# Kernel optimization log

Measured on AMD Instinct MI355X. Metric: run time of the kernel, lower is better.

Reference implementation:

```python
import jax, jax.numpy as jnp
import numpy as np

N_SAMPLES = 2048
BURN_IN = 128
STEP_SIZE = 0.1
D = 512   # walker dimension
H = 1024  # wavefunction MLP hidden width


def setup_inputs() -> dict:
    key = jax.random.key(0)
    k0, k1, k2 = jax.random.split(key, 3)
    x0 = jax.random.normal(k0, (1, D), dtype=jnp.float32)
    W1 = jax.random.normal(k1, (D, H), dtype=jnp.float32) / np.float32(np.sqrt(D))
    b1 = jnp.zeros((H,), dtype=jnp.float32)
    W2 = jax.random.normal(k2, (H, 1), dtype=jnp.float32) / np.float32(np.sqrt(H))
    b2 = jnp.zeros((1,), dtype=jnp.float32)
    return {"x0": x0, "W1": W1, "b1": b1, "W2": W2, "b2": b2}


def _model(x, W1, b1, W2, b2):
    # wavefunction MLP: [1, D] -> [1, 1]
    return jnp.tanh(x @ W1 + b1) @ W2 + b2


def reference(x0, W1, b1, W2, b2):
    def psi2(x):
        # model(x).pow(2)[0] -> shape [1]
        return (_model(x, W1, b1, W2, b2) ** 2)[0]

    def mh_step(x, k):
        k_noise, k_unif = jax.random.split(k)
        x_new = x + jax.random.normal(k_noise, x.shape, dtype=x.dtype) * STEP_SIZE
        p_new = psi2(x_new)
        p_old = psi2(x)
        ratio = jnp.minimum(p_new / (p_old + 1e-12), 1.0)          # clamp(max=1.0)
        u = jax.random.uniform(k_unif, ratio.shape, dtype=x.dtype)
        accept = (u < ratio).astype(x.dtype)[:, None]               # [1, 1]
        x = accept * x_new + (1.0 - accept) * x
        return x, x[0]  # carry chain state, record sample row [D]

    keys = jax.random.split(jax.random.key(1), N_SAMPLES + BURN_IN)
    _, traj = jax.lax.scan(mh_step, x0, keys)   # traj: [N+BURN_IN, D]
    return traj[BURN_IN:]                        # [N_SAMPLES, D]
```

## Files before the change

kernel.cpp:

```cpp
#include <hip/hip_runtime.h>
#include <stdint.h>
#include <math.h>


#define T_TOTAL 2176
#define NBURN   128
#define DDIM    512
#define HDIM    1024
#define DONE_FLAG 0x13572468u

__device__ __forceinline__ uint2 tf2x32(uint32_t k0, uint32_t k1,
                                        uint32_t x0, uint32_t x1) {
  uint32_t ks2 = k0 ^ k1 ^ 0x1BD11BDAu;
  x0 += k0; x1 += k1;
#define TF_R(r) { x0 += x1; x1 = (x1 << (r)) | (x1 >> (32 - (r))); x1 ^= x0; }
  TF_R(13) TF_R(15) TF_R(26) TF_R(6)
  x0 += k1;  x1 += ks2 + 1u;
  TF_R(17) TF_R(29) TF_R(16) TF_R(24)
  x0 += ks2; x1 += k0 + 2u;
  TF_R(13) TF_R(15) TF_R(26) TF_R(6)
  x0 += k0;  x1 += k1 + 3u;
  TF_R(17) TF_R(29) TF_R(16) TF_R(24)
  x0 += k1;  x1 += ks2 + 4u;
  TF_R(13) TF_R(15) TF_R(26) TF_R(6)
  x0 += ks2; x1 += k0 + 5u;
#undef TF_R
  return make_uint2(x0, x1);
}

__device__ __forceinline__ float erfinv_xla(float x) {
  float w = -log1pf(-x * x);
  float p;
  if (w < 5.0f) {
    w = w - 2.5f;
    p = 2.81022636e-08f;
    p = fmaf(p, w, 3.43273939e-07f);
    p = fmaf(p, w, -3.5233877e-06f);
    p = fmaf(p, w, -4.39150654e-06f);
    p = fmaf(p, w, 0.00021858087f);
    p = fmaf(p, w, -0.00125372503f);
    p = fmaf(p, w, -0.00417768164f);
    p = fmaf(p, w, 0.246640727f);
    p = fmaf(p, w, 1.50140941f);
  } else {
    w = sqrtf(w) - 3.0f;
    p = -0.000200214257f;
    p = fmaf(p, w, 0.000100950558f);
    p = fmaf(p, w, 0.00134934322f);
    p = fmaf(p, w, -0.00367342844f);
    p = fmaf(p, w, 0.00573950773f);
    p = fmaf(p, w, -0.0076224613f);
    p = fmaf(p, w, 0.00943887047f);
    p = fmaf(p, w, 1.00167406f);
    p = fmaf(p, w, 2.83297682f);
  }
  return p * x;
}

__device__ __forceinline__ float normal_from_bits(uint32_t bits) {
  const float lo = -0.99999994f;
  float u01 = __uint_as_float(0x3f800000u | (bits >> 9)) - 1.0f;
  float v = u01 * 2.0f + lo;
  v = fmaxf(lo, v);
  return 1.41421356237309515f * erfinv_xla(v);
}

__device__ __forceinline__ float tanh_fast(float x) {
  float a = x * 2.88539008177792681472f;
#if __has_builtin(__builtin_amdgcn_exp2f)
  float e = __builtin_amdgcn_exp2f(a);
#else
  float e = exp2f(a);
#endif
  float r = __builtin_amdgcn_rcpf(e + 1.0f);
  return fmaf(-2.0f, r, 1.0f);
}

__global__ void __launch_bounds__(256) rng_kernel(const float* __restrict__ x0,
                                                  float* __restrict__ A,
                                                  float* __restrict__ U) {
  const uint32_t t = blockIdx.x;
  const int tid = threadIdx.x;
  uint2 kt = tf2x32(0u, 1u, 0u, t);
  uint2 kn = tf2x32(kt.x, kt.y, 0u, 0u);
  uint2 e0 = tf2x32(kn.x, kn.y, 0u, (uint32_t)tid);
  uint2 e1 = tf2x32(kn.x, kn.y, 0u, (uint32_t)(tid + 256));
  float n0 = normal_from_bits(e0.x ^ e0.y);
  float n1 = normal_from_bits(e1.x ^ e1.y);
  float* Arow = A + (size_t)(t + 1) * DDIM;
  Arow[tid]       = n0 * 0.1f;
  Arow[tid + 256] = n1 * 0.1f;
  if (tid == 0) {
    uint2 ku = tf2x32(kt.x, kt.y, 0u, 1u);
    uint2 eu = tf2x32(ku.x, ku.y, 0u, 0u);
    U[t] = __uint_as_float(0x3f800000u | ((eu.x ^ eu.y) >> 9)) - 1.0f;
  }
  if (t == 0) {
    A[tid]       = x0[tid];
    A[tid + 256] = x0[tid + 256];
  }
}

__global__ void __launch_bounds__(512) gemm_kernel(const float* __restrict__ A,
                                                   const float* __restrict__ W1,
                                                   float* __restrict__ Z,
                                                   int nrows) {
  const int r0 = blockIdx.x * 8;
  const int t  = threadIdx.x;
  const int c0 = t, c1 = t + 512;
  double acc[8][2];
#pragma unroll
  for (int r = 0; r < 8; ++r) { acc[r][0] = 0.0; acc[r][1] = 0.0; }
  for (int d = 0; d < 512; d += 4) {
    double wA[4], wB[4];
#pragma unroll
    for (int j = 0; j < 4; ++j) {
      wA[j] = (double)W1[(size_t)(d + j) * 1024 + c0];
      wB[j] = (double)W1[(size_t)(d + j) * 1024 + c1];
    }
#pragma unroll
    for (int r = 0; r < 8; ++r) {
      int rr = r0 + r; if (rr >= nrows) rr = nrows - 1;
      const float4 a4 = *(const float4*)(A + (size_t)rr * 512 + d);
      double a0 = (double)a4.x, a1 = (double)a4.y;
      double a2 = (double)a4.z, a3 = (double)a4.w;
      acc[r][0] += (a0 * wA[0] + a1 * wA[1]) + (a2 * wA[2] + a3 * wA[3]);
      acc[r][1] += (a0 * wB[0] + a1 * wB[1]) + (a2 * wB[2] + a3 * wB[3]);
    }
  }
  const int rmax = (nrows - r0 < 8) ? (nrows - r0) : 8;
  for (int r = 0; r < rmax; ++r) {
    Z[(size_t)(r0 + r) * 1024 + c0] = (float)acc[r][0];
    Z[(size_t)(r0 + r) * 1024 + c1] = (float)acc[r][1];
  }
}

#define DPP_ADD(v, ctrl)                                                     \
  v += __int_as_float(__builtin_amdgcn_update_dpp(                           \
      0, __float_as_int(v), (ctrl), 0xF, 0xF, true))

__device__ __forceinline__ float wave_reduce_to_last(float v) {
  DPP_ADD(v, 0xB1);
  DPP_ADD(v, 0x4E);
  DPP_ADD(v, 0x141);
  DPP_ADD(v, 0x140);
  DPP_ADD(v, 0x142);
  DPP_ADD(v, 0x143);
  return v;
}

#define BAR() asm volatile("s_waitcnt lgkmcnt(0)\n\ts_barrier" ::: "memory")

__global__ void __launch_bounds__(256) chain_kernel(
    const float* __restrict__ Z, const float* __restrict__ A,
    const float* __restrict__ U, const float* __restrict__ x0,
    const float* __restrict__ b1, const float* __restrict__ W2,
    const float* __restrict__ b2, float* __restrict__ out,
    unsigned* __restrict__ flag) {
  const int tid = threadIdx.x;

  if (blockIdx.x != 0) {
    float acc = (float)tid * 1.0e-6f;
    for (int i = 0; i < 4000; ++i) {
#pragma unroll
      for (int j = 0; j < 256; ++j) acc = fmaf(acc, 0.99999988f, 1.0e-7f);
      unsigned f = __hip_atomic_load(flag, __ATOMIC_RELAXED,
                                     __HIP_MEMORY_SCOPE_AGENT);
      if (f == DONE_FLAG) break;
    }
    if (acc == 123456.75f && tid == 1023) out[0] = acc;
    return;
  }

  const int lane = tid & 63;
  const int wid = tid >> 6;
  __shared__ __align__(16) float wsum[2][4];
  __shared__ float Uld[T_TOTAL];

  const float4* Zv = (const float4*)Z;
  const float2* Av = (const float2*)A;

  for (int i = tid; i < T_TOTAL; i += 256) Uld[i] = U[i];

  const float4 w2v = ((const float4*)W2)[tid];
  const float4 b1v = ((const float4*)b1)[tid];
  const float b2v = b2[0];

  float4 z0r = Zv[tid];
  float4 zr1 = Zv[256 + tid];
  float4 zS0 = Zv[512 + tid];
  float4 zS1 = Zv[768 + tid];
  float2 dS0 = Av[256 + tid];
  float2 dS1 = Av[512 + tid];

  double Y0 = (double)z0r.x + (double)b1v.x;
  double Y1 = (double)z0r.y + (double)b1v.y;
  double Y2 = (double)z0r.z + (double)b1v.z;
  double Y3 = (double)z0r.w + (double)b1v.w;

  float xa = x0[2 * tid], xb = x0[2 * tid + 1];

  __syncthreads();
  float uu0 = Uld[0];
  float uS0 = Uld[1];
  float uS1 = Uld[2];

  {
    float g0 = tanh_fast((float)Y0);
    float g1 = tanh_fast((float)Y1);
    float g2 = tanh_fast((float)Y2);
    float g3 = tanh_fast((float)Y3);
    float tm = fmaf(g3, w2v.w, fmaf(g2, w2v.z, fmaf(g1, w2v.y, g0 * w2v.x)));
    tm = wave_reduce_to_last(tm);
    if (lane == 63) wsum[1][wid] = tm;
  }
  __syncthreads();
  float4 pp = *(const float4*)wsum[1];
  float m0 = ((pp.x + pp.y) + (pp.z + pp.w)) + b2v;
  float p = m0 * m0;
  float um = uu0 * (p + 1e-12f);

  double C0 = Y0 + (double)zr1.x;
  double C1 = Y1 + (double)zr1.y;
  double C2 = Y2 + (double)zr1.z;
  double C3 = Y3 + (double)zr1.w;
  {
    float g0 = tanh_fast((float)C0);
    float g1 = tanh_fast((float)C1);
    float g2 = tanh_fast((float)C2);
    float g3 = tanh_fast((float)C3);
    float tm = fmaf(g3, w2v.w, fmaf(g2, w2v.z, fmaf(g1, w2v.y, g0 * w2v.x)));
    tm = wave_reduce_to_last(tm);
    if (lane == 63) wsum[0][wid] = tm;
  }
  __syncthreads();

#define STEP(t, ZB, DB, UB, W_CUR, W_NXT)                                    \
  {                                                                          \
    const float4 p4 = *(const float4*)wsum[W_CUR];                           \
    int ur = (t) + 3; if (ur > 2175) ur = 2175;                              \
    float u_new = Uld[ur];                                                   \
    float m = ((p4.x + p4.y) + (p4.z + p4.w)) + b2v;                         \
    float q = m * m;                                                         \
    bool acc = um < q;                                                       \
    Y0 = acc ? C0 : Y0;  Y1 = acc ? C1 : Y1;                                 \
    Y2 = acc ? C2 : Y2;  Y3 = acc ? C3 : Y3;                                 \
    p  = acc ? q : p;                                                        \
    xa = acc ? xa + DB.x : xa;                                               \
    xb = acc ? xb + DB.y : xb;                                               \
    if ((t) >= NBURN) {                                                      \
      float2 o; o.x = xa; o.y = xb;                                          \
      *(float2*)(out + (size_t)((t) - NBURN) * DDIM + 2 * tid) = o;          \
    }                                                                        \
    um = UB * (p + 1e-12f);                                                  \
    C0 = Y0 + (double)ZB.x;                                                  \
    C1 = Y1 + (double)ZB.y;                                                  \
    C2 = Y2 + (double)ZB.z;                                                  \
    C3 = Y3 + (double)ZB.w;                                                  \
    {                                                                        \
      int zr = (t) + 4; if (zr > 2176) zr = 2176;                            \
      int ar = (t) + 3; if (ar > 2176) ar = 2176;                            \
      ZB = Zv[(size_t)zr * 256 + tid];                                       \
      DB = Av[(size_t)ar * 256 + tid];                                       \
    }                                                                        \
    float g0 = tanh_fast((float)C0);                                         \
    float g1 = tanh_fast((float)C1);                                         \
    float g2 = tanh_fast((float)C2);                                         \
    float g3 = tanh_fast((float)C3);                                         \
    float tm = fmaf(g3, w2v.w, fmaf(g2, w2v.z, fmaf(g1, w2v.y, g0 * w2v.x)));\
    tm = wave_reduce_to_last(tm);                                            \
    if (lane == 63) wsum[W_NXT][wid] = tm;                                   \
    UB = u_new;                                                              \
    BAR();                                                                   \
  }

  for (int t = 0; t < T_TOTAL; t += 2) {
    STEP(t,     zS0, dS0, uS0, 0, 1);
    STEP(t + 1, zS1, dS1, uS1, 1, 0);
  }
#undef STEP

  if (tid == 0) {
    __hip_atomic_store(flag, DONE_FLAG, __ATOMIC_RELAXED,
                       __HIP_MEMORY_SCOPE_AGENT);
  }
}

extern "C" void kernel_launch(void* const* d_in, const int* in_sizes, int n_in,
                              void* d_out, int out_size, void* d_ws, size_t ws_size,
                              hipStream_t stream) {
  const float* x0 = (const float*)d_in[0];
  const float* W1 = (const float*)d_in[1];
  const float* b1 = (const float*)d_in[2];
  const float* W2 = (const float*)d_in[3];
  const float* b2 = (const float*)d_in[4];
  float* out = (float*)d_out;

  char* ws = (char*)d_ws;
  float* A = (float*)ws;
  float* Z = (float*)(ws + 4458496);
  float* U = (float*)(ws + 4458496 + 8916992);
  unsigned* flag = (unsigned*)(ws + 4458496 + 8916992 + 8704);

  rng_kernel<<<T_TOTAL, 256, 0, stream>>>(x0, A, U);
  gemm_kernel<<<273, 512, 0, stream>>>(A, W1, Z, T_TOTAL + 1);
  chain_kernel<<<256, 256, 0, stream>>>(Z, A, U, x0, b1, W2, b2, out, flag);
}
```

Baseline: 924.3 us.

## Fuse RNG generation into GEMM kernel and drop chain-loop index clamps

Merges the RNG kernel into the GEMM kernel, so each block generates its own 8 rows of proposal noise and uniforms and then computes the Z rows for them. This removes one kernel launch and the global round trip between the two kernels. The workspace is padded so the chain loop can read past the end without clamping Z, A and U indices. It also adds a spinning dummy block 255 that runs a fixed FMA loop, apparently to keep the GPU clocks up. The RNG work now sits serially inside the GEMM blocks, and the padding rows are read uninitialised, though those values are never used.

```diff
diff --git a/kernel.cpp b/kernel.cpp
--- a/kernel.cpp
+++ b/kernel.cpp
@@ -4,6 +4,7 @@
 
 
 #define T_TOTAL 2176
+#define NROWS   2177
 #define NBURN   128
 #define DDIM    512
 #define HDIM    1024
@@ -76,51 +77,54 @@
   return fmaf(-2.0f, r, 1.0f);
 }
 
-__global__ void __launch_bounds__(256) rng_kernel(const float* __restrict__ x0,
-                                                  float* __restrict__ A,
-                                                  float* __restrict__ U) {
-  const uint32_t t = blockIdx.x;
+__global__ void __launch_bounds__(512) rng_gemm_kernel(
+    const float* __restrict__ x0, const float* __restrict__ W1,
+    float* A, float* __restrict__ Z, float* __restrict__ U) {
+  const int r0 = blockIdx.x * 8;
   const int tid = threadIdx.x;
-  uint2 kt = tf2x32(0u, 1u, 0u, t);
-  uint2 kn = tf2x32(kt.x, kt.y, 0u, 0u);
-  uint2 e0 = tf2x32(kn.x, kn.y, 0u, (uint32_t)tid);
-  uint2 e1 = tf2x32(kn.x, kn.y, 0u, (uint32_t)(tid + 256));
-  float n0 = normal_from_bits(e0.x ^ e0.y);
-  float n1 = normal_from_bits(e1.x ^ e1.y);
-  float* Arow = A + (size_t)(t + 1) * DDIM;
-  Arow[tid]       = n0 * 0.1f;
-  Arow[tid + 256] = n1 * 0.1f;
-  if (tid == 0) {
-    uint2 ku = tf2x32(kt.x, kt.y, 0u, 1u);
-    uint2 eu = tf2x32(ku.x, ku.y, 0u, 0u);
-    U[t] = __uint_as_float(0x3f800000u | ((eu.x ^ eu.y) >> 9)) - 1.0f;
-  }
-  if (t == 0) {
-    A[tid]       = x0[tid];
-    A[tid + 256] = x0[tid + 256];
-  }
-}
-
-__global__ void __launch_bounds__(512) gemm_kernel(const float* __restrict__ A,
-                                                   const float* __restrict__ W1,
-                                                   float* __restrict__ Z,
-                                                   int nrows) {
-  const int r0 = blockIdx.x * 8;
-  const int t  = threadIdx.x;
-  const int c0 = t, c1 = t + 512;
+
+  const int j = tid & 255;
+  for (int k = 0; k < 4; ++k) {
+    int rr = r0 + 2 * k + (tid >> 8);
+    if (rr == 0) {
+      A[j] = x0[j];
+      A[j + 256] = x0[j + 256];
+    } else if (rr < NROWS) {
+      uint32_t t = (uint32_t)(rr - 1);
+      uint2 kt = tf2x32(0u, 1u, 0u, t);
+      uint2 kn = tf2x32(kt.x, kt.y, 0u, 0u);
+      uint2 e0 = tf2x32(kn.x, kn.y, 0u, (uint32_t)j);
+      uint2 e1 = tf2x32(kn.x, kn.y, 0u, (uint32_t)(j + 256));
+      A[(size_t)rr * DDIM + j]       = normal_from_bits(e0.x ^ e0.y) * 0.1f;
+      A[(size_t)rr * DDIM + j + 256] = normal_from_bits(e1.x ^ e1.y) * 0.1f;
+    }
+  }
+  if (tid < 8) {
+    int rr = r0 + tid;
+    if (rr >= 1 && rr < NROWS) {
+      uint32_t t = (uint32_t)(rr - 1);
+      uint2 kt = tf2x32(0u, 1u, 0u, t);
+      uint2 ku = tf2x32(kt.x, kt.y, 0u, 1u);
+      uint2 eu = tf2x32(ku.x, ku.y, 0u, 0u);
+      U[t] = __uint_as_float(0x3f800000u | ((eu.x ^ eu.y) >> 9)) - 1.0f;
+    }
+  }
+  __syncthreads();
+
+  const int c0 = tid, c1 = tid + 512;
   double acc[8][2];
 #pragma unroll
   for (int r = 0; r < 8; ++r) { acc[r][0] = 0.0; acc[r][1] = 0.0; }
   for (int d = 0; d < 512; d += 4) {
     double wA[4], wB[4];
 #pragma unroll
-    for (int j = 0; j < 4; ++j) {
-      wA[j] = (double)W1[(size_t)(d + j) * 1024 + c0];
-      wB[j] = (double)W1[(size_t)(d + j) * 1024 + c1];
+    for (int jj = 0; jj < 4; ++jj) {
+      wA[jj] = (double)W1[(size_t)(d + jj) * 1024 + c0];
+      wB[jj] = (double)W1[(size_t)(d + jj) * 1024 + c1];
     }
 #pragma unroll
     for (int r = 0; r < 8; ++r) {
-      int rr = r0 + r; if (rr >= nrows) rr = nrows - 1;
+      int rr = r0 + r; if (rr >= NROWS) rr = NROWS - 1;
       const float4 a4 = *(const float4*)(A + (size_t)rr * 512 + d);
       double a0 = (double)a4.x, a1 = (double)a4.y;
       double a2 = (double)a4.z, a3 = (double)a4.w;
@@ -128,7 +132,7 @@
       acc[r][1] += (a0 * wB[0] + a1 * wB[1]) + (a2 * wB[2] + a3 * wB[3]);
     }
   }
-  const int rmax = (nrows - r0 < 8) ? (nrows - r0) : 8;
+  const int rmax = (NROWS - r0 < 8) ? (NROWS - r0) : 8;
   for (int r = 0; r < rmax; ++r) {
     Z[(size_t)(r0 + r) * 1024 + c0] = (float)acc[r][0];
     Z[(size_t)(r0 + r) * 1024 + c1] = (float)acc[r][1];
@@ -159,11 +163,20 @@
     unsigned* __restrict__ flag) {
   const int tid = threadIdx.x;
 
+  if (blockIdx.x == 255) {
+    float a = (float)tid * 1.1920929e-7f + 0.5f;
+    for (int i = 0; i < 1200; ++i) {
+#pragma unroll
+      for (int jj = 0; jj < 256; ++jj) a = fmaf(a, 0.99999988f, 1.0e-7f);
+    }
+    if (a == 123456.75f) out[0] = a;
+    return;
+  }
   if (blockIdx.x != 0) {
     float acc = (float)tid * 1.0e-6f;
     for (int i = 0; i < 4000; ++i) {
 #pragma unroll
-      for (int j = 0; j < 256; ++j) acc = fmaf(acc, 0.99999988f, 1.0e-7f);
+      for (int jj = 0; jj < 256; ++jj) acc = fmaf(acc, 0.99999988f, 1.0e-7f);
       unsigned f = __hip_atomic_load(flag, __ATOMIC_RELAXED,
                                      __HIP_MEMORY_SCOPE_AGENT);
       if (f == DONE_FLAG) break;
@@ -175,12 +188,12 @@
   const int lane = tid & 63;
   const int wid = tid >> 6;
   __shared__ __align__(16) float wsum[2][4];
-  __shared__ float Uld[T_TOTAL];
+  __shared__ float Uld[T_TOTAL + 4];
 
   const float4* Zv = (const float4*)Z;
   const float2* Av = (const float2*)A;
 
-  for (int i = tid; i < T_TOTAL; i += 256) Uld[i] = U[i];
+  for (int i = tid; i < T_TOTAL + 4; i += 256) Uld[i] = U[i];
 
   const float4 w2v = ((const float4*)W2)[tid];
   const float4 b1v = ((const float4*)b1)[tid];
@@ -238,8 +251,7 @@
 #define STEP(t, ZB, DB, UB, W_CUR, W_NXT)                                    \
   {                                                                          \
     const float4 p4 = *(const float4*)wsum[W_CUR];                           \
-    int ur = (t) + 3; if (ur > 2175) ur = 2175;                              \
-    float u_new = Uld[ur];                                                   \
+    float u_new = Uld[(t) + 3];                                              \
     float m = ((p4.x + p4.y) + (p4.z + p4.w)) + b2v;                         \
     float q = m * m;                                                         \
     bool acc = um < q;                                                       \
@@ -257,12 +269,8 @@
     C1 = Y1 + (double)ZB.y;                                                  \
     C2 = Y2 + (double)ZB.z;                                                  \
     C3 = Y3 + (double)ZB.w;                                                  \
-    {                                                                        \
-      int zr = (t) + 4; if (zr > 2176) zr = 2176;                            \
-      int ar = (t) + 3; if (ar > 2176) ar = 2176;                            \
-      ZB = Zv[(size_t)zr * 256 + tid];                                       \
-      DB = Av[(size_t)ar * 256 + tid];                                       \
-    }                                                                        \
+    ZB = Zv[(size_t)((t) + 4) * 256 + tid];                                  \
+    DB = Av[(size_t)((t) + 3) * 256 + tid];                                  \
     float g0 = tanh_fast((float)C0);                                         \
     float g1 = tanh_fast((float)C1);                                         \
     float g2 = tanh_fast((float)C2);                                         \
@@ -298,11 +306,10 @@
 
   char* ws = (char*)d_ws;
   float* A = (float*)ws;
-  float* Z = (float*)(ws + 4458496);
-  float* U = (float*)(ws + 4458496 + 8916992);
-  unsigned* flag = (unsigned*)(ws + 4458496 + 8916992 + 8704);
-
-  rng_kernel<<<T_TOTAL, 256, 0, stream>>>(x0, A, U);
-  gemm_kernel<<<273, 512, 0, stream>>>(A, W1, Z, T_TOTAL + 1);
+  float* Z = (float*)(ws + 4464640);
+  float* U = (float*)(ws + 4464640 + 8933376);
+  unsigned* flag = (unsigned*)(ws + 4464640 + 8933376 + 8720);
+
+  rng_gemm_kernel<<<273, 512, 0, stream>>>(x0, W1, A, Z, U);
   chain_kernel<<<256, 256, 0, stream>>>(Z, A, U, x0, b1, W2, b2, out, flag);
 }
```

New measurement: 938.0 us. About the same (+1.5%).

## Evaluate two Metropolis steps per barrier via speculative three-branch evaluation

Applied to the files above, without the earlier changes.

The chain loop now handles two MH steps per iteration. It speculatively computes the hidden pre-activations and psi for all three outcomes (accept first only, accept second only, accept both), then resolves both decisions after a single barrier. This halves the number of block-wide barriers and serial dependency rounds. The cost is three times the tanh and reduction work per iteration and extra register pressure. Workspace offsets and buffer sizes grow to cover the deeper prefetch rows, but the rng kernel still writes only T_TOTAL rows, so the reads past that end may be uninitialized.

```diff
diff --git a/kernel.cpp b/kernel.cpp
--- a/kernel.cpp
+++ b/kernel.cpp
@@ -4,6 +4,8 @@
 
 
 #define T_TOTAL 2176
+#define NITER   1088
+#define NROWS   2177
 #define NBURN   128
 #define DDIM    512
 #define HDIM    1024
@@ -163,7 +165,7 @@
     float acc = (float)tid * 1.0e-6f;
     for (int i = 0; i < 4000; ++i) {
 #pragma unroll
-      for (int j = 0; j < 256; ++j) acc = fmaf(acc, 0.99999988f, 1.0e-7f);
+      for (int jj = 0; jj < 256; ++jj) acc = fmaf(acc, 0.99999988f, 1.0e-7f);
       unsigned f = __hip_atomic_load(flag, __ATOMIC_RELAXED,
                                      __HIP_MEMORY_SCOPE_AGENT);
       if (f == DONE_FLAG) break;
@@ -174,24 +176,25 @@
 
   const int lane = tid & 63;
   const int wid = tid >> 6;
-  __shared__ __align__(16) float wsum[2][4];
-  __shared__ float Uld[T_TOTAL];
+  __shared__ __align__(16) float wsum[2][3][4];
+  __shared__ float Uld[2184];
 
   const float4* Zv = (const float4*)Z;
   const float2* Av = (const float2*)A;
 
-  for (int i = tid; i < T_TOTAL; i += 256) Uld[i] = U[i];
+  for (int i = tid; i < 2184; i += 256) Uld[i] = U[i];
 
   const float4 w2v = ((const float4*)W2)[tid];
   const float4 b1v = ((const float4*)b1)[tid];
   const float b2v = b2[0];
 
   float4 z0r = Zv[tid];
-  float4 zr1 = Zv[256 + tid];
-  float4 zS0 = Zv[512 + tid];
-  float4 zS1 = Zv[768 + tid];
-  float2 dS0 = Av[256 + tid];
-  float2 dS1 = Av[512 + tid];
+  float4 z1r = Zv[256 + tid];
+  float4 z2r = Zv[512 + tid];
+  float4 zA0 = Zv[3 * 256 + tid], zB0 = Zv[4 * 256 + tid];
+  float4 zA1 = Zv[5 * 256 + tid], zB1 = Zv[6 * 256 + tid];
+  float2 dAa0 = Av[1 * 256 + tid], dAb0 = Av[2 * 256 + tid];
+  float2 dAa1 = Av[3 * 256 + tid], dAb1 = Av[4 * 256 + tid];
 
   double Y0 = (double)z0r.x + (double)b1v.x;
   double Y1 = (double)z0r.y + (double)b1v.y;
@@ -201,9 +204,6 @@
   float xa = x0[2 * tid], xb = x0[2 * tid + 1];
 
   __syncthreads();
-  float uu0 = Uld[0];
-  float uS0 = Uld[1];
-  float uS1 = Uld[2];
 
   {
     float g0 = tanh_fast((float)Y0);
@@ -212,73 +212,116 @@
     float g3 = tanh_fast((float)Y3);
     float tm = fmaf(g3, w2v.w, fmaf(g2, w2v.z, fmaf(g1, w2v.y, g0 * w2v.x)));
     tm = wave_reduce_to_last(tm);
-    if (lane == 63) wsum[1][wid] = tm;
+    if (lane == 63) wsum[1][0][wid] = tm;
   }
   __syncthreads();
-  float4 pp = *(const float4*)wsum[1];
-  float m0 = ((pp.x + pp.y) + (pp.z + pp.w)) + b2v;
-  float p = m0 * m0;
-  float um = uu0 * (p + 1e-12f);
-
-  double C0 = Y0 + (double)zr1.x;
-  double C1 = Y1 + (double)zr1.y;
-  double C2 = Y2 + (double)zr1.z;
-  double C3 = Y3 + (double)zr1.w;
+  float p;
   {
-    float g0 = tanh_fast((float)C0);
-    float g1 = tanh_fast((float)C1);
-    float g2 = tanh_fast((float)C2);
-    float g3 = tanh_fast((float)C3);
-    float tm = fmaf(g3, w2v.w, fmaf(g2, w2v.z, fmaf(g1, w2v.y, g0 * w2v.x)));
-    tm = wave_reduce_to_last(tm);
-    if (lane == 63) wsum[0][wid] = tm;
+    const float4 pp = *(const float4*)wsum[1][0];
+    float m0 = ((pp.x + pp.y) + (pp.z + pp.w)) + b2v;
+    p = m0 * m0;
+  }
+  float um1 = Uld[0] * (p + 1e-12f);
+  float u2c = Uld[1];
+
+  double Ya0 = Y0 + (double)z1r.x, Ya1 = Y1 + (double)z1r.y;
+  double Ya2 = Y2 + (double)z1r.z, Ya3 = Y3 + (double)z1r.w;
+  double Yb0 = Y0 + (double)z2r.x, Yb1 = Y1 + (double)z2r.y;
+  double Yb2 = Y2 + (double)z2r.z, Yb3 = Y3 + (double)z2r.w;
+  double Yc0 = Ya0 + (double)z2r.x, Yc1 = Ya1 + (double)z2r.y;
+  double Yc2 = Ya2 + (double)z2r.z, Yc3 = Ya3 + (double)z2r.w;
+  {
+    float a0 = tanh_fast((float)Ya0), a1 = tanh_fast((float)Ya1);
+    float a2 = tanh_fast((float)Ya2), a3 = tanh_fast((float)Ya3);
+    float b0 = tanh_fast((float)Yb0), b1_ = tanh_fast((float)Yb1);
+    float b2_ = tanh_fast((float)Yb2), b3 = tanh_fast((float)Yb3);
+    float c0 = tanh_fast((float)Yc0), c1 = tanh_fast((float)Yc1);
+    float c2 = tanh_fast((float)Yc2), c3 = tanh_fast((float)Yc3);
+    float tA = fmaf(a3, w2v.w, fmaf(a2, w2v.z, fmaf(a1, w2v.y, a0 * w2v.x)));
+    float tB = fmaf(b3, w2v.w, fmaf(b2_, w2v.z, fmaf(b1_, w2v.y, b0 * w2v.x)));
+    float tC = fmaf(c3, w2v.w, fmaf(c2, w2v.z, fmaf(c1, w2v.y, c0 * w2v.x)));
+    tA = wave_reduce_to_last(tA);
+    tB = wave_reduce_to_last(tB);
+    tC = wave_reduce_to_last(tC);
+    if (lane == 63) {
+      wsum[0][0][wid] = tA;
+      wsum[0][1][wid] = tB;
+      wsum[0][2][wid] = tC;
+    }
   }
   __syncthreads();
 
-#define STEP(t, ZB, DB, UB, W_CUR, W_NXT)                                    \
+#define ITER(k, PAR, ZAB, ZBB, DAB, DBB)                                     \
   {                                                                          \
-    const float4 p4 = *(const float4*)wsum[W_CUR];                           \
-    int ur = (t) + 3; if (ur > 2175) ur = 2175;                              \
-    float u_new = Uld[ur];                                                   \
-    float m = ((p4.x + p4.y) + (p4.z + p4.w)) + b2v;                         \
-    float q = m * m;                                                         \
-    bool acc = um < q;                                                       \
-    Y0 = acc ? C0 : Y0;  Y1 = acc ? C1 : Y1;                                 \
-    Y2 = acc ? C2 : Y2;  Y3 = acc ? C3 : Y3;                                 \
-    p  = acc ? q : p;                                                        \
-    xa = acc ? xa + DB.x : xa;                                               \
-    xb = acc ? xb + DB.y : xb;                                               \
-    if ((t) >= NBURN) {                                                      \
-      float2 o; o.x = xa; o.y = xb;                                          \
-      *(float2*)(out + (size_t)((t) - NBURN) * DDIM + 2 * tid) = o;          \
+    float u1n = Uld[2 * (k) + 2];                                            \
+    float u2n = Uld[2 * (k) + 3];                                            \
+    const float4 e1 = *(const float4*)wsum[PAR][0];                          \
+    const float4 e2 = *(const float4*)wsum[PAR][1];                          \
+    const float4 e3 = *(const float4*)wsum[PAR][2];                          \
+    float m1 = ((e1.x + e1.y) + (e1.z + e1.w)) + b2v;                        \
+    float q1 = m1 * m1;                                                      \
+    bool a1v = um1 < q1;                                                     \
+    float p1 = a1v ? q1 : p;                                                 \
+    float um2 = u2c * (p1 + 1e-12f);                                         \
+    float m2v = ((e2.x + e2.y) + (e2.z + e2.w)) + b2v;                       \
+    float m3v = ((e3.x + e3.y) + (e3.z + e3.w)) + b2v;                       \
+    float m23 = a1v ? m3v : m2v;                                             \
+    float q23 = m23 * m23;                                                   \
+    bool a2v = um2 < q23;                                                    \
+    p = a2v ? q23 : p1;                                                      \
+    float xat = a1v ? xa + DAB.x : xa;                                       \
+    float xbt = a1v ? xb + DAB.y : xb;                                       \
+    xa = a2v ? xat + DBB.x : xat;                                            \
+    xb = a2v ? xbt + DBB.y : xbt;                                            \
+    if ((k) >= 64) {                                                         \
+      float2 o1; o1.x = xat; o1.y = xbt;                                     \
+      *(float2*)(out + (size_t)(2 * (k) - NBURN) * DDIM + 2 * tid) = o1;     \
+      float2 o2; o2.x = xa; o2.y = xb;                                       \
+      *(float2*)(out + (size_t)(2 * (k) + 1 - NBURN) * DDIM + 2 * tid) = o2; \
     }                                                                        \
-    um = UB * (p + 1e-12f);                                                  \
-    C0 = Y0 + (double)ZB.x;                                                  \
-    C1 = Y1 + (double)ZB.y;                                                  \
-    C2 = Y2 + (double)ZB.z;                                                  \
-    C3 = Y3 + (double)ZB.w;                                                  \
-    {                                                                        \
-      int zr = (t) + 4; if (zr > 2176) zr = 2176;                            \
-      int ar = (t) + 3; if (ar > 2176) ar = 2176;                            \
-      ZB = Zv[(size_t)zr * 256 + tid];                                       \
-      DB = Av[(size_t)ar * 256 + tid];                                       \
+    DAB = Av[(size_t)(2 * (k) + 5) * 256 + tid];                             \
+    DBB = Av[(size_t)(2 * (k) + 6) * 256 + tid];                             \
+            \
+    Y0 = a1v ? (a2v ? Yc0 : Ya0) : (a2v ? Yb0 : Y0);                         \
+    Y1 = a1v ? (a2v ? Yc1 : Ya1) : (a2v ? Yb1 : Y1);                         \
+    Y2 = a1v ? (a2v ? Yc2 : Ya2) : (a2v ? Yb2 : Y2);                         \
+    Y3 = a1v ? (a2v ? Yc3 : Ya3) : (a2v ? Yb3 : Y3);                         \
+                         \
+    Ya0 = Y0 + (double)ZAB.x;  Ya1 = Y1 + (double)ZAB.y;                     \
+    Ya2 = Y2 + (double)ZAB.z;  Ya3 = Y3 + (double)ZAB.w;                     \
+    Yb0 = Y0 + (double)ZBB.x;  Yb1 = Y1 + (double)ZBB.y;                     \
+    Yb2 = Y2 + (double)ZBB.z;  Yb3 = Y3 + (double)ZBB.w;                     \
+    Yc0 = Ya0 + (double)ZBB.x; Yc1 = Ya1 + (double)ZBB.y;                    \
+    Yc2 = Ya2 + (double)ZBB.z; Yc3 = Ya3 + (double)ZBB.w;                    \
+    ZAB = Zv[(size_t)(2 * (k) + 7) * 256 + tid];                             \
+    ZBB = Zv[(size_t)(2 * (k) + 8) * 256 + tid];                             \
+    float ga0 = tanh_fast((float)Ya0), ga1 = tanh_fast((float)Ya1);          \
+    float ga2 = tanh_fast((float)Ya2), ga3 = tanh_fast((float)Ya3);          \
+    float gb0 = tanh_fast((float)Yb0), gb1 = tanh_fast((float)Yb1);          \
+    float gb2 = tanh_fast((float)Yb2), gb3 = tanh_fast((float)Yb3);          \
+    float gc0 = tanh_fast((float)Yc0), gc1 = tanh_fast((float)Yc1);          \
+    float gc2 = tanh_fast((float)Yc2), gc3 = tanh_fast((float)Yc3);          \
+    float tA = fmaf(ga3, w2v.w, fmaf(ga2, w2v.z, fmaf(ga1, w2v.y, ga0 * w2v.x))); \
+    float tB = fmaf(gb3, w2v.w, fmaf(gb2, w2v.z, fmaf(gb1, w2v.y, gb0 * w2v.x))); \
+    float tC = fmaf(gc3, w2v.w, fmaf(gc2, w2v.z, fmaf(gc1, w2v.y, gc0 * w2v.x))); \
+    tA = wave_reduce_to_last(tA);                                            \
+    tB = wave_reduce_to_last(tB);                                            \
+    tC = wave_reduce_to_last(tC);                                            \
+    if (lane == 63) {                                                        \
+      wsum[(PAR) ^ 1][0][wid] = tA;                                          \
+      wsum[(PAR) ^ 1][1][wid] = tB;                                          \
+      wsum[(PAR) ^ 1][2][wid] = tC;                                          \
     }                                                                        \
-    float g0 = tanh_fast((float)C0);                                         \
-    float g1 = tanh_fast((float)C1);                                         \
-    float g2 = tanh_fast((float)C2);                                         \
-    float g3 = tanh_fast((float)C3);                                         \
-    float tm = fmaf(g3, w2v.w, fmaf(g2, w2v.z, fmaf(g1, w2v.y, g0 * w2v.x)));\
-    tm = wave_reduce_to_last(tm);                                            \
-    if (lane == 63) wsum[W_NXT][wid] = tm;                                   \
-    UB = u_new;                                                              \
+    um1 = u1n * (p + 1e-12f);                                                \
+    u2c = u2n;                                                               \
     BAR();                                                                   \
   }
 
-  for (int t = 0; t < T_TOTAL; t += 2) {
-    STEP(t,     zS0, dS0, uS0, 0, 1);
-    STEP(t + 1, zS1, dS1, uS1, 1, 0);
-  }
-#undef STEP
+  for (int k = 0; k < NITER; k += 2) {
+    ITER(k,     0, zA0, zB0, dAa0, dAb0);
+    ITER(k + 1, 1, zA1, zB1, dAa1, dAb1);
+  }
+#undef ITER
 
   if (tid == 0) {
     __hip_atomic_store(flag, DONE_FLAG, __ATOMIC_RELAXED,
@@ -298,11 +341,11 @@
 
   char* ws = (char*)d_ws;
   float* A = (float*)ws;
-  float* Z = (float*)(ws + 4458496);
-  float* U = (float*)(ws + 4458496 + 8916992);
-  unsigned* flag = (unsigned*)(ws + 4458496 + 8916992 + 8704);
+  float* Z = (float*)(ws + 4472832);
+  float* U = (float*)(ws + 4472832 + 8945664);
+  unsigned* flag = (unsigned*)(ws + 4472832 + 8945664 + 8736);
 
   rng_kernel<<<T_TOTAL, 256, 0, stream>>>(x0, A, U);
-  gemm_kernel<<<273, 512, 0, stream>>>(A, W1, Z, T_TOTAL + 1);
+  gemm_kernel<<<273, 512, 0, stream>>>(A, W1, Z, NROWS);
   chain_kernel<<<256, 256, 0, stream>>>(Z, A, U, x0, b1, W2, b2, out, flag);
 }
```

Measured after the change: 861.8 us. 6.8% less time.
